# Kernel optimization log

Measured on AMD Instinct MI355X. Metric: run time of the kernel, lower is better.

The kernel has to match this reference:

```python
import jax, jax.numpy as jnp
import numpy as np

N_NODES = 50000
N_EDGES = 800000
D = 128


def setup_inputs() -> dict:
    key = jax.random.key(0)
    ks = jax.random.split(key, 6)
    stdv = 1.0 / np.sqrt(D)
    inputs = {
        "input": jax.random.normal(ks[0], (N_NODES, D), dtype=jnp.float32),
        "h0": jax.random.normal(ks[1], (N_NODES, D), dtype=jnp.float32),
        # COO representation of the (normalized) sparse adjacency
        "vals": jax.random.uniform(ks[2], (N_EDGES,), dtype=jnp.float32) / 16.0,
        "weight": jax.random.uniform(ks[3], (D, D), dtype=jnp.float32, minval=-stdv, maxval=stdv),
        "lamda": jnp.float32(0.5),
        "alpha": jnp.float32(0.1),
        "row": jax.random.randint(ks[4], (N_EDGES,), 0, N_NODES),
        "col": jax.random.randint(ks[5], (N_EDGES,), 0, N_NODES),
        "l": 4,
    }
    return inputs


def reference(input, h0, vals, weight, lamda, alpha, row, col, l):
    # theta = log(lamda / l + 1)
    theta = jnp.log(lamda / l + 1.0)
    # hi = spmm(adj, input): gather source-node features, scale by edge
    # values, scatter-add into destination rows.  [E, D] -> [N, D]
    hi = jax.ops.segment_sum(vals[:, None] * input[col], row, num_segments=input.shape[0])
    # variant=False path
    support = (1.0 - alpha) * hi + alpha * h0
    r = support
    # output = theta * support @ W + (1 - theta) * r
    output = theta * jnp.matmul(support, weight) + (1.0 - theta) * r
    return output
```

## Files before the change

kernel.cpp:

```cpp
#include <hip/hip_runtime.h>
#include <cmath>

constexpr int N_NODES = 50000;
constexpr int N_EDGES = 800000;
constexpr int D = 128;
constexpr int CAP = 32;
constexpr int OVF_CAP = 8192;
constexpr int CNT_STRIDE = 16;

constexpr int EPB = 2048;
constexpr int SCAT_BLOCKS = (N_EDGES + EPB - 1) / EPB;
constexpr int CAST_BLOCKS = (N_NODES * D / 8 + 255) / 256;

constexpr size_t OFF_OVFCNT = 3200000;
constexpr size_t OFF_BUCKET = 3200064;
constexpr size_t OFF_OVF    = 9600064;
constexpr size_t OFF_PACKED = 9731136;
constexpr size_t OFF_WT     = 22531136;

typedef __attribute__((ext_vector_type(8))) short bf16x8;
typedef __attribute__((ext_vector_type(4))) float f32x4;

__device__ __forceinline__ unsigned bf16rn(float f) {
    unsigned u = __float_as_uint(f);
    return (u + 0x7fffu + ((u >> 16) & 1u)) >> 16;
}
__device__ __forceinline__ float bf_lo(unsigned u) { return __uint_as_float(u << 16); }
__device__ __forceinline__ float bf_hi(unsigned u) { return __uint_as_float(u & 0xffff0000u); }

__device__ __forceinline__ unsigned enc_val(float v) {
    int m = (int)(v * 1048576.0f + 0.5f);
    if (m > 65535) m = 65535;
    if (m < 0) m = 0;
    return (unsigned)m;
}

__device__ __forceinline__ void push_edge(
    int r, int c, float v,
    int* __restrict__ cnt, unsigned* __restrict__ bucket,
    int* __restrict__ ovf_cnt, int4* __restrict__ ovf)
{
    unsigned ent = (unsigned)c | (enc_val(v) << 16);
    int pos = atomicAdd(&cnt[(size_t)r * CNT_STRIDE], 1);
    if (pos < CAP) bucket[(size_t)r * CAP + pos] = ent;
    else {
        int o = atomicAdd(ovf_cnt, 1);
        if (o < OVF_CAP) ovf[o] = make_int4(r, c, __float_as_int(v), 0);
    }
}

__global__ __launch_bounds__(256) void scatter_cast(
    const int* __restrict__ row, const int* __restrict__ col,
    const float* __restrict__ vals, const float* __restrict__ input,
    const float* __restrict__ weight,
    int* __restrict__ cnt, unsigned* __restrict__ bucket,
    int* __restrict__ ovf_cnt, int4* __restrict__ ovf,
    unsigned* __restrict__ packed, ushort* __restrict__ wt)
{
    if (blockIdx.x < SCAT_BLOCKS) {
        const int gbase = blockIdx.x * (EPB / 4);
        #pragma unroll
        for (int it = 0; it < EPB / 4 / 256; ++it) {
            int gi = gbase + it * 256 + threadIdx.x;
            if (gi >= N_EDGES / 4) break;
            int4   r4 = ((const int4*)row)[gi];
            int4   c4 = ((const int4*)col)[gi];
            float4 v4 = ((const float4*)vals)[gi];
            push_edge(r4.x, c4.x, v4.x, cnt, bucket, ovf_cnt, ovf);
            push_edge(r4.y, c4.y, v4.y, cnt, bucket, ovf_cnt, ovf);
            push_edge(r4.z, c4.z, v4.z, cnt, bucket, ovf_cnt, ovf);
            push_edge(r4.w, c4.w, v4.w, cnt, bucket, ovf_cnt, ovf);
        }
    } else if (blockIdx.x < SCAT_BLOCKS + CAST_BLOCKS) {
        int i = (blockIdx.x - SCAT_BLOCKS) * 256 + threadIdx.x;
        if (i >= N_NODES * D / 8) return;
        const float4* f = (const float4*)(input + (size_t)i * 8);
        float4 a = f[0], b = f[1];
        uint4 o;
        o.x = bf16rn(a.x) | (bf16rn(a.y) << 16);
        o.y = bf16rn(a.z) | (bf16rn(a.w) << 16);
        o.z = bf16rn(b.x) | (bf16rn(b.y) << 16);
        o.w = bf16rn(b.z) | (bf16rn(b.w) << 16);
        ((uint4*)packed)[i] = o;
    } else {
        #pragma unroll
        for (int j = 0; j < 64; ++j) {
            int idx = threadIdx.x + j * 256;
            int k = idx >> 7, n = idx & 127;
            wt[n * 128 + k] = (ushort)bf16rn(weight[idx]);
        }
    }
}

__global__ __launch_bounds__(256) void gather_support(
    const unsigned* __restrict__ packed,
    const float* __restrict__ h0,
    const float* __restrict__ alpha_p,
    const int* __restrict__ cnt,
    const unsigned* __restrict__ bucket,
    const int* __restrict__ ovf_cnt_p,
    const int4* __restrict__ ovf,
    float* __restrict__ support)
{
    const float alpha = *alpha_p;
    const float oma = 1.0f - alpha;
    const int wv   = threadIdx.x >> 6;
    const int lane = threadIdx.x & 63;
    const int q    = lane & 15;
    const int slot = lane >> 4;

    const int g = blockIdx.x * 4 + wv;
    if (g >= N_NODES) return;

    int n = cnt[(size_t)g * CNT_STRIDE];
    int novf = *ovf_cnt_p;
    if (novf > OVF_CAP) novf = OVF_CAP;
    if (n > CAP) n = CAP;
    const unsigned* b = bucket + (size_t)g * CAP;
    const uint4* pk = (const uint4*)packed;

    const int q4 = (n + 3) >> 2;
    const int s0 = slot * q4;
    int s1 = s0 + q4; if (s1 > n) s1 = n;

    float acc[8] = {0.f, 0.f, 0.f, 0.f, 0.f, 0.f, 0.f, 0.f};
    for (int e = s0; e < s1; e += 4) {
        int rem = s1 - e;
        unsigned m0 = b[e];
        unsigned m1 = (rem > 1) ? b[e + 1] : 0u;
        unsigned m2 = (rem > 2) ? b[e + 2] : 0u;
        unsigned m3 = (rem > 3) ? b[e + 3] : 0u;
        uint4 x0 = pk[(size_t)(m0 & 0xffffu) * 16 + q];
        uint4 x1 = pk[(size_t)(m1 & 0xffffu) * 16 + q];
        uint4 x2 = pk[(size_t)(m2 & 0xffffu) * 16 + q];
        uint4 x3 = pk[(size_t)(m3 & 0xffffu) * 16 + q];
        float v0 = (float)(m0 >> 16) * (1.0f / 1048576.0f);
        float v1 = (float)(m1 >> 16) * (1.0f / 1048576.0f);
        float v2 = (float)(m2 >> 16) * (1.0f / 1048576.0f);
        float v3 = (float)(m3 >> 16) * (1.0f / 1048576.0f);
        acc[0] += v0 * bf_lo(x0.x); acc[1] += v0 * bf_hi(x0.x);
        acc[2] += v0 * bf_lo(x0.y); acc[3] += v0 * bf_hi(x0.y);
        acc[4] += v0 * bf_lo(x0.z); acc[5] += v0 * bf_hi(x0.z);
        acc[6] += v0 * bf_lo(x0.w); acc[7] += v0 * bf_hi(x0.w);
        acc[0] += v1 * bf_lo(x1.x); acc[1] += v1 * bf_hi(x1.x);
        acc[2] += v1 * bf_lo(x1.y); acc[3] += v1 * bf_hi(x1.y);
        acc[4] += v1 * bf_lo(x1.z); acc[5] += v1 * bf_hi(x1.z);
        acc[6] += v1 * bf_lo(x1.w); acc[7] += v1 * bf_hi(x1.w);
        acc[0] += v2 * bf_lo(x2.x); acc[1] += v2 * bf_hi(x2.x);
        acc[2] += v2 * bf_lo(x2.y); acc[3] += v2 * bf_hi(x2.y);
        acc[4] += v2 * bf_lo(x2.z); acc[5] += v2 * bf_hi(x2.z);
        acc[6] += v2 * bf_lo(x2.w); acc[7] += v2 * bf_hi(x2.w);
        acc[0] += v3 * bf_lo(x3.x); acc[1] += v3 * bf_hi(x3.x);
        acc[2] += v3 * bf_lo(x3.y); acc[3] += v3 * bf_hi(x3.y);
        acc[4] += v3 * bf_lo(x3.z); acc[5] += v3 * bf_hi(x3.z);
        acc[6] += v3 * bf_lo(x3.w); acc[7] += v3 * bf_hi(x3.w);
    }
    #pragma unroll
    for (int j = 0; j < 8; ++j) {
        acc[j] += __shfl_xor(acc[j], 16);
        acc[j] += __shfl_xor(acc[j], 32);
    }
    if (slot == 0) {
        for (int o = 0; o < novf; ++o) {
            int4 mm = ovf[o];
            if (mm.x == g) {
                float v = __int_as_float(mm.z);
                uint4 x = pk[(size_t)mm.y * 16 + q];
                acc[0] += v * bf_lo(x.x); acc[1] += v * bf_hi(x.x);
                acc[2] += v * bf_lo(x.y); acc[3] += v * bf_hi(x.y);
                acc[4] += v * bf_lo(x.z); acc[5] += v * bf_hi(x.z);
                acc[6] += v * bf_lo(x.w); acc[7] += v * bf_hi(x.w);
            }
        }
        const float* hp = h0 + (size_t)g * D + q * 8;
        float4 ha = *(const float4*)(hp);
        float4 hb = *(const float4*)(hp + 4);
        float* sp = support + (size_t)g * D + q * 8;
        float4 sa, sb;
        sa.x = oma * acc[0] + alpha * ha.x;
        sa.y = oma * acc[1] + alpha * ha.y;
        sa.z = oma * acc[2] + alpha * ha.z;
        sa.w = oma * acc[3] + alpha * ha.w;
        sb.x = oma * acc[4] + alpha * hb.x;
        sb.y = oma * acc[5] + alpha * hb.y;
        sb.z = oma * acc[6] + alpha * hb.z;
        sb.w = oma * acc[7] + alpha * hb.w;
        *(float4*)(sp) = sa;
        *(float4*)(sp + 4) = sb;
    }
}

__global__ __launch_bounds__(256) void gemm_mfma(
    const ushort* __restrict__ wt,
    const float* __restrict__ lamda_p,
    const int* __restrict__ l_p,
    float* __restrict__ data)
{
    constexpr int SP = 136;
    __shared__ ushort sA[64 * SP];
    __shared__ ushort sB[128 * SP];

    const int tid = threadIdx.x;
    const float lamda = *lamda_p;
    const float theta = logf(lamda / (float)(*l_p) + 1.0f);
    const float omt = 1.0f - theta;
    const int row0 = blockIdx.x * 64;

    #pragma unroll
    for (int j = 0; j < 8; ++j) {
        int idx = j * 256 + tid;
        int n  = idx >> 4;
        int k8 = (idx & 15) << 3;
        *(uint4*)(&sB[n * SP + k8]) = ((const uint4*)wt)[idx];
    }
    #pragma unroll
    for (int j = 0; j < 8; ++j) {
        int idx = j * 256 + tid;
        int rr = idx >> 5;
        int c4 = (idx & 31) << 2;
        int g = row0 + rr;
        float4 s = make_float4(0.f, 0.f, 0.f, 0.f);
        if (g < N_NODES) s = *(const float4*)(data + (size_t)g * D + c4);
        uint2 pkv;
        pkv.x = bf16rn(s.x) | (bf16rn(s.y) << 16);
        pkv.y = bf16rn(s.z) | (bf16rn(s.w) << 16);
        *(uint2*)(&sA[rr * SP + c4]) = pkv;
    }
    __syncthreads();

    const int wave = tid >> 6;
    const int lane = tid & 63;
    const int m    = lane & 15;
    const int quad = lane >> 4;
    const int arow = wave * 16 + m;

    f32x4 acc[8] = {};
    #pragma unroll
    for (int kb = 0; kb < 4; ++kb) {
        bf16x8 a = *(const bf16x8*)(&sA[arow * SP + kb * 32 + quad * 8]);
        #pragma unroll
        for (int nt = 0; nt < 8; ++nt) {
            bf16x8 b = *(const bf16x8*)(&sB[(nt * 16 + m) * SP + kb * 32 + quad * 8]);
            acc[nt] = __builtin_amdgcn_mfma_f32_16x16x32_bf16(a, b, acc[nt], 0, 0, 0);
        }
    }

    const int gbase = row0 + wave * 16 + quad * 4;
    #pragma unroll
    for (int nt = 0; nt < 8; ++nt) {
        int colb = nt * 16 + m;
        #pragma unroll
        for (int i = 0; i < 4; ++i) {
            int g = gbase + i;
            if (g < N_NODES) {
                size_t off = (size_t)g * D + colb;
                float s = data[off];
                data[off] = theta * acc[nt][i] + omt * s;
            }
        }
    }
}

extern "C" void kernel_launch(void* const* d_in, const int* in_sizes, int n_in,
                              void* d_out, int out_size, void* d_ws, size_t ws_size,
                              hipStream_t stream) {
    const float* input  = (const float*)d_in[0];
    const float* h0     = (const float*)d_in[1];
    const float* vals   = (const float*)d_in[2];
    const float* weight = (const float*)d_in[3];
    const float* lamda  = (const float*)d_in[4];
    const float* alpha  = (const float*)d_in[5];
    const int*   row    = (const int*)d_in[6];
    const int*   col    = (const int*)d_in[7];
    const int*   l      = (const int*)d_in[8];
    float* out = (float*)d_out;

    char* ws = (char*)d_ws;
    int*      cnt     = (int*)ws;
    int*      ovf_cnt = (int*)(ws + OFF_OVFCNT);
    unsigned* bucket  = (unsigned*)(ws + OFF_BUCKET);
    int4*     ovf     = (int4*)(ws + OFF_OVF);
    unsigned* packed  = (unsigned*)(ws + OFF_PACKED);
    ushort*   wt      = (ushort*)(ws + OFF_WT);

    hipMemsetAsync(ws, 0, OFF_BUCKET, stream);

    scatter_cast<<<SCAT_BLOCKS + CAST_BLOCKS + 1, 256, 0, stream>>>(
        row, col, vals, input, weight, cnt, bucket, ovf_cnt, ovf, packed, wt);

    int gatherb = (N_NODES + 3) / 4;
    gather_support<<<gatherb, 256, 0, stream>>>(
        packed, h0, alpha, cnt, bucket, ovf_cnt, ovf, out);

    int gemmb = (N_NODES + 63) / 64;
    gemm_mfma<<<gemmb, 256, 0, stream>>>(wt, lamda, l, out);
}
```

Baseline: 204.6 us.

## Replace global per-row atomic scatter with two-level bin sort into LDS buckets

Edges are first binned by row range into 256 coarse queues, using a block-local histogram, a scan, and one global atomic per bin per block. A new kernel then builds the per-row buckets in shared memory and writes them out contiguously. This removes roughly 800K global atomics on padded per-row counters, and the memset no longer has to clear the large strided count array. In exchange it adds a kernel launch, an extra pass through the queue in global memory, and a queue capacity limit that falls back to the overflow path.

Result: faster. 188.7 us (-7.8%).

```diff
diff --git a/kernel.cpp b/kernel.cpp
--- a/kernel.cpp
+++ b/kernel.cpp
@@ -6,17 +6,22 @@
 constexpr int D = 128;
 constexpr int CAP = 32;
 constexpr int OVF_CAP = 8192;
-constexpr int CNT_STRIDE = 16;
-
-constexpr int EPB = 2048;
-constexpr int SCAT_BLOCKS = (N_EDGES + EPB - 1) / EPB;
+
+constexpr int NBIN = 256;
+constexpr int RPP  = 196;
+constexpr int QCAP = 4096;
+constexpr int QCNT_STRIDE = 16;
+constexpr int EPB_BIN = 4096;
+constexpr int BIN_BLOCKS = (N_EDGES + EPB_BIN - 1) / EPB_BIN;
 constexpr int CAST_BLOCKS = (N_NODES * D / 8 + 255) / 256;
 
-constexpr size_t OFF_OVFCNT = 3200000;
-constexpr size_t OFF_BUCKET = 3200064;
-constexpr size_t OFF_OVF    = 9600064;
-constexpr size_t OFF_PACKED = 9731136;
-constexpr size_t OFF_WT     = 22531136;
+constexpr size_t OFF_OVFCNT = 16384;
+constexpr size_t OFF_QUEUE  = 16448;
+constexpr size_t OFF_CNT    = 8405056;
+constexpr size_t OFF_BUCKET = 8605056;
+constexpr size_t OFF_OVF    = 15005056;
+constexpr size_t OFF_PACKED = 15136128;
+constexpr size_t OFF_WT     = 27936128;
 
 typedef __attribute__((ext_vector_type(8))) short bf16x8;
 typedef __attribute__((ext_vector_type(4))) float f32x4;
@@ -35,44 +40,78 @@
     return (unsigned)m;
 }
 
-__device__ __forceinline__ void push_edge(
-    int r, int c, float v,
-    int* __restrict__ cnt, unsigned* __restrict__ bucket,
-    int* __restrict__ ovf_cnt, int4* __restrict__ ovf)
-{
-    unsigned ent = (unsigned)c | (enc_val(v) << 16);
-    int pos = atomicAdd(&cnt[(size_t)r * CNT_STRIDE], 1);
-    if (pos < CAP) bucket[(size_t)r * CAP + pos] = ent;
-    else {
-        int o = atomicAdd(ovf_cnt, 1);
-        if (o < OVF_CAP) ovf[o] = make_int4(r, c, __float_as_int(v), 0);
-    }
-}
-
-__global__ __launch_bounds__(256) void scatter_cast(
+__global__ __launch_bounds__(256) void binsort_cast(
     const int* __restrict__ row, const int* __restrict__ col,
     const float* __restrict__ vals, const float* __restrict__ input,
     const float* __restrict__ weight,
-    int* __restrict__ cnt, unsigned* __restrict__ bucket,
+    int* __restrict__ qcnt, uint2* __restrict__ queue,
     int* __restrict__ ovf_cnt, int4* __restrict__ ovf,
     unsigned* __restrict__ packed, ushort* __restrict__ wt)
 {
-    if (blockIdx.x < SCAT_BLOCKS) {
-        const int gbase = blockIdx.x * (EPB / 4);
-        #pragma unroll
-        for (int it = 0; it < EPB / 4 / 256; ++it) {
-            int gi = gbase + it * 256 + threadIdx.x;
-            if (gi >= N_EDGES / 4) break;
-            int4   r4 = ((const int4*)row)[gi];
-            int4   c4 = ((const int4*)col)[gi];
-            float4 v4 = ((const float4*)vals)[gi];
-            push_edge(r4.x, c4.x, v4.x, cnt, bucket, ovf_cnt, ovf);
-            push_edge(r4.y, c4.y, v4.y, cnt, bucket, ovf_cnt, ovf);
-            push_edge(r4.z, c4.z, v4.z, cnt, bucket, ovf_cnt, ovf);
-            push_edge(r4.w, c4.w, v4.w, cnt, bucket, ovf_cnt, ovf);
-        }
-    } else if (blockIdx.x < SCAT_BLOCKS + CAST_BLOCKS) {
-        int i = (blockIdx.x - SCAT_BLOCKS) * 256 + threadIdx.x;
+    __shared__ uint2 lq[EPB_BIN];
+    __shared__ int hist[NBIN], scn[NBIN], off[NBIN], gbase[NBIN], fill[NBIN];
+
+    const int tid = threadIdx.x;
+    if (blockIdx.x < BIN_BLOCKS) {
+        int er[16]; unsigned ec[16];
+        const int gi0 = blockIdx.x * (EPB_BIN / 4);
+        #pragma unroll
+        for (int it = 0; it < 4; ++it) {
+            int gi = gi0 + it * 256 + tid;
+            int4 r4 = make_int4(-1, -1, -1, -1);
+            int4 c4 = make_int4(0, 0, 0, 0);
+            float4 v4 = make_float4(0.f, 0.f, 0.f, 0.f);
+            if (gi < N_EDGES / 4) {
+                r4 = ((const int4*)row)[gi];
+                c4 = ((const int4*)col)[gi];
+                v4 = ((const float4*)vals)[gi];
+            }
+            er[it*4+0] = r4.x; ec[it*4+0] = (unsigned)c4.x | (enc_val(v4.x) << 16);
+            er[it*4+1] = r4.y; ec[it*4+1] = (unsigned)c4.y | (enc_val(v4.y) << 16);
+            er[it*4+2] = r4.z; ec[it*4+2] = (unsigned)c4.z | (enc_val(v4.z) << 16);
+            er[it*4+3] = r4.w; ec[it*4+3] = (unsigned)c4.w | (enc_val(v4.w) << 16);
+        }
+        hist[tid] = 0;
+        __syncthreads();
+        #pragma unroll
+        for (int j = 0; j < 16; ++j)
+            if (er[j] >= 0) atomicAdd(&hist[er[j] / RPP], 1);
+        __syncthreads();
+        scn[tid] = hist[tid];
+        __syncthreads();
+        for (int s = 1; s < NBIN; s <<= 1) {
+            int t = (tid >= s) ? scn[tid - s] : 0;
+            __syncthreads();
+            scn[tid] += t;
+            __syncthreads();
+        }
+        off[tid]   = scn[tid] - hist[tid];
+        gbase[tid] = atomicAdd(&qcnt[tid * QCNT_STRIDE], hist[tid]);
+        fill[tid]  = 0;
+        __syncthreads();
+        #pragma unroll
+        for (int j = 0; j < 16; ++j)
+            if (er[j] >= 0) {
+                int b = er[j] / RPP;
+                int p = atomicAdd(&fill[b], 1);
+                lq[off[b] + p] = make_uint2(ec[j], (unsigned)er[j]);
+            }
+        __syncthreads();
+        const int total = scn[NBIN - 1];
+        for (int i = tid; i < total; i += 256) {
+            uint2 e = lq[i];
+            int r = (int)e.y;
+            int b = r / RPP;
+            int dst = gbase[b] + (i - off[b]);
+            if (dst < QCAP) queue[(size_t)b * QCAP + dst] = e;
+            else {
+                int o = atomicAdd(ovf_cnt, 1);
+                if (o < OVF_CAP) ovf[o] = make_int4(r, (int)(e.x & 0xffffu),
+                    __float_as_int((float)(e.x >> 16) * (1.0f / 1048576.0f)), 0);
+            }
+        }
+    } else if (blockIdx.x < BIN_BLOCKS + CAST_BLOCKS) {
+        int i = (blockIdx.x - BIN_BLOCKS) * 256 + tid;
         if (i >= N_NODES * D / 8) return;
         const float4* f = (const float4*)(input + (size_t)i * 8);
         float4 a = f[0], b = f[1];
@@ -85,10 +124,49 @@
     } else {
         #pragma unroll
         for (int j = 0; j < 64; ++j) {
-            int idx = threadIdx.x + j * 256;
+            int idx = tid + j * 256;
             int k = idx >> 7, n = idx & 127;
             wt[n * 128 + k] = (ushort)bf16rn(weight[idx]);
         }
+    }
+}
+
+__global__ __launch_bounds__(256) void bucket_build(
+    const uint2* __restrict__ queue, const int* __restrict__ qcnt,
+    int* __restrict__ ovf_cnt, int4* __restrict__ ovf,
+    int* __restrict__ cnt, unsigned* __restrict__ bucket)
+{
+    __shared__ int cl[RPP];
+    __shared__ unsigned lb[RPP * CAP];
+
+    const int b = blockIdx.x;
+    const int tid = threadIdx.x;
+    if (tid < RPP) cl[tid] = 0;
+    __syncthreads();
+
+    int nb = qcnt[b * QCNT_STRIDE];
+    if (nb > QCAP) nb = QCAP;
+    for (int i = tid; i < nb; i += 256) {
+        uint2 e = queue[(size_t)b * QCAP + i];
+        int r  = (int)e.y;
+        int rl = r - b * RPP;
+        int pos = atomicAdd(&cl[rl], 1);
+        if (pos < CAP) lb[rl * CAP + pos] = e.x;
+        else {
+            int o = atomicAdd(ovf_cnt, 1);
+            if (o < OVF_CAP) ovf[o] = make_int4(r, (int)(e.x & 0xffffu),
+                __float_as_int((float)(e.x >> 16) * (1.0f / 1048576.0f)), 0);
+        }
+    }
+    __syncthreads();
+
+    if (tid < RPP) {
+        int r = b * RPP + tid;
+        if (r < N_NODES) cnt[r] = cl[tid];
+    }
+    for (int i = tid; i < RPP * CAP; i += 256) {
+        int gidx = b * RPP * CAP + i;
+        if (gidx < N_NODES * CAP) bucket[gidx] = lb[i];
     }
 }
 
@@ -112,7 +190,7 @@
     const int g = blockIdx.x * 4 + wv;
     if (g >= N_NODES) return;
 
-    int n = cnt[(size_t)g * CNT_STRIDE];
+    int n = cnt[g];
     int novf = *ovf_cnt_p;
     if (novf > OVF_CAP) novf = OVF_CAP;
     if (n > CAP) n = CAP;
@@ -276,17 +354,21 @@
     float* out = (float*)d_out;
 
     char* ws = (char*)d_ws;
-    int*      cnt     = (int*)ws;
+    int*      qcnt    = (int*)ws;
     int*      ovf_cnt = (int*)(ws + OFF_OVFCNT);
+    uint2*    queue   = (uint2*)(ws + OFF_QUEUE);
+    int*      cnt     = (int*)(ws + OFF_CNT);
     unsigned* bucket  = (unsigned*)(ws + OFF_BUCKET);
     int4*     ovf     = (int4*)(ws + OFF_OVF);
     unsigned* packed  = (unsigned*)(ws + OFF_PACKED);
     ushort*   wt      = (ushort*)(ws + OFF_WT);
 
-    hipMemsetAsync(ws, 0, OFF_BUCKET, stream);
-
-    scatter_cast<<<SCAT_BLOCKS + CAST_BLOCKS + 1, 256, 0, stream>>>(
-        row, col, vals, input, weight, cnt, bucket, ovf_cnt, ovf, packed, wt);
+    hipMemsetAsync(ws, 0, OFF_QUEUE, stream);
+
+    binsort_cast<<<BIN_BLOCKS + CAST_BLOCKS + 1, 256, 0, stream>>>(
+        row, col, vals, input, weight, qcnt, queue, ovf_cnt, ovf, packed, wt);
+
+    bucket_build<<<NBIN, 256, 0, stream>>>(queue, qcnt, ovf_cnt, ovf, cnt, bucket);
 
     int gatherb = (N_NODES + 3) / 4;
     gather_support<<<gatherb, 256, 0, stream>>>(
```
